# Optimization experiments

Measured on AMD Instinct MI355X. Metric: run time of the kernel, lower is better.

The kernel has to match this reference:

```python
import jax, jax.numpy as jnp
from jax import lax
import numpy as np

# ---- config (matches init_kwargs) ----
B, T, D_IN = 4, 2048, 513
NC = D_IN - 1                 # neural channels
N_DAYS, N_CLASSES = 24, 41
PATCH, STRIDE = 14, 4
T_OUT = (T - PATCH) // STRIDE + 1   # 509
D_MODEL = 512                 # n_units
PROJ = 4096
L = 5                         # n_layers
DSTATE, DCONV, HEADDIM = 64, 4, 64
DI = 2 * D_MODEL              # expand=2 -> d_inner
H = DI // HEADDIM             # 16 heads
CONVD = DI + 2 * DSTATE       # conv channels (x,B,C)
DINPROJ = 2 * DI + 2 * DSTATE + H
NM = 2 * L                    # fwd+bwd Mamba instances
EPS = 1e-5


def setup_inputs() -> dict:
    key = jax.random.key(0)
    ks = jax.random.split(key, 16)
    s = 0.02
    x = jax.random.normal(ks[0], (B, T, D_IN), jnp.float32)
    day_idx = jax.random.randint(ks[1], (B,), 0, N_DAYS)
    day_w = jnp.eye(NC)[None] + s * jax.random.normal(ks[2], (N_DAYS, NC, NC), jnp.float32)
    day_b = s * jax.random.normal(ks[3], (N_DAYS, NC), jnp.float32)
    w1 = s * jax.random.normal(ks[4], (PROJ, D_IN * PATCH), jnp.float32)
    b1 = jnp.zeros((PROJ,), jnp.float32)
    w2 = s * jax.random.normal(ks[5], (D_MODEL, PROJ), jnp.float32)
    b2 = jnp.zeros((D_MODEL,), jnp.float32)
    ln_w = jnp.ones((L, D_MODEL), jnp.float32)
    ln_b = jnp.zeros((L, D_MODEL), jnp.float32)
    m_in_w = s * jax.random.normal(ks[6], (NM, DINPROJ, D_MODEL), jnp.float32)
    m_conv_w = s * jax.random.normal(ks[7], (NM, CONVD, DCONV), jnp.float32)
    m_conv_b = jnp.zeros((NM, CONVD), jnp.float32)
    dt = jax.random.uniform(ks[8], (NM, H), jnp.float32, 0.025, 1.0)
    m_dt = jnp.log(jnp.expm1(dt)) + 1.0          # dt_bias with +1 short-memory bias
    m_Alog = jnp.tile(jnp.log(jnp.arange(1, H + 1, dtype=jnp.float32))[None], (NM, 1))
    m_D = jnp.ones((NM, H), jnp.float32)
    m_norm_w = jnp.ones((NM, DI), jnp.float32)
    m_out_w = s * jax.random.normal(ks[9], (NM, D_MODEL, DI), jnp.float32)
    out_w = s * jax.random.normal(ks[10], (N_CLASSES, D_MODEL), jnp.float32)
    out_b = jnp.zeros((N_CLASSES,), jnp.float32)
    return dict(x=x, day_idx=day_idx, day_w=day_w, day_b=day_b, w1=w1, b1=b1,
                w2=w2, b2=b2, ln_w=ln_w, ln_b=ln_b, m_in_w=m_in_w, m_conv_w=m_conv_w,
                m_conv_b=m_conv_b, m_dt=m_dt, m_Alog=m_Alog, m_D=m_D,
                m_norm_w=m_norm_w, m_out_w=m_out_w, out_w=out_w, out_b=out_b)


def _layernorm(x, w, b):
    mu = jnp.mean(x, -1, keepdims=True)
    v = jnp.mean((x - mu) ** 2, -1, keepdims=True)
    return (x - mu) * lax.rsqrt(v + EPS) * w + b


def _mamba2(x, in_w, conv_w, conv_b, dt_bias, A_log, Dp, norm_w, out_w):
    """Mamba2 forward: x [B,T,Dm] -> [B,T,Dm]. Sequential selective scan."""
    Bn, Tn, _ = x.shape
    zxbcdt = x @ in_w.T                                   # [B,T,DINPROJ]
    z = zxbcdt[..., :DI]
    xBC = zxbcdt[..., DI:DI + CONVD]
    dt = jax.nn.softplus(zxbcdt[..., DI + CONVD:] + dt_bias)  # [B,T,H]
    # causal depthwise conv over time
    xc = jnp.transpose(xBC, (0, 2, 1))                    # [B,C,T]
    xc = lax.conv_general_dilated(xc, conv_w[:, None, :], (1,), [(DCONV - 1, 0)],
                                  feature_group_count=CONVD)
    xBC = jax.nn.silu(jnp.transpose(xc, (0, 2, 1)) + conv_b)
    xs = xBC[..., :DI].reshape(Bn, Tn, H, HEADDIM)        # [B,T,H,P]
    Bm = xBC[..., DI:DI + DSTATE]                         # [B,T,N] (ngroups=1)
    Cm = xBC[..., DI + DSTATE:]                           # [B,T,N]
    A = -jnp.exp(A_log)                                   # [H]
    dA = jnp.exp(dt * A)                                  # [B,T,H]

    def step(h, inp):
        xt, bt, ct, dat, dtt = inp                        # [B,H,P],[B,N],[B,N],[B,H],[B,H]
        h = h * dat[:, :, None, None] + (dtt[:, :, None] * xt)[..., None] * bt[:, None, None, :]
        y = jnp.einsum('bhpn,bn->bhp', h, ct)
        return h, y

    h0 = jnp.zeros((Bn, H, HEADDIM, DSTATE), x.dtype)
    xsT = jnp.moveaxis(xs, 1, 0)
    _, ys = lax.scan(step, h0, (xsT, jnp.moveaxis(Bm, 1, 0), jnp.moveaxis(Cm, 1, 0),
                                jnp.moveaxis(dA, 1, 0), jnp.moveaxis(dt, 1, 0)))
    y = jnp.moveaxis(ys, 0, 1) + Dp[None, None, :, None] * xs
    y = y.reshape(Bn, Tn, DI)
    y = y * jax.nn.silu(z)                                # gated RMSNorm
    y = y * lax.rsqrt(jnp.mean(y * y, -1, keepdims=True) + EPS) * norm_w
    return y @ out_w.T


def reference(x, day_idx, day_w, day_b, w1, b1, w2, b2, ln_w, ln_b,
              m_in_w, m_conv_w, m_conv_b, m_dt, m_Alog, m_D, m_norm_w, m_out_w,
              out_w, out_b):
    xn, xt = x[..., :-1], x[..., -1:]
    W = day_w[day_idx]                                    # [B,NC,NC]
    bsel = day_b[day_idx][:, None, :]
    xn = jnp.einsum('btd,bdk->btk', xn, W) + bsel
    xn = xn / (1.0 + jnp.abs(xn))                         # Softsign
    h = jnp.concatenate([xn, xt], -1)                     # [B,T,D_IN]
    # patch unfold: [B,T_OUT,PATCH,D_IN] -> [B,T_OUT,PATCH*D_IN]
    idx = jnp.arange(T_OUT)[:, None] * STRIDE + jnp.arange(PATCH)[None, :]
    h = h[:, idx, :].reshape(B, T_OUT, PATCH * D_IN)
    # input projection with Softsign
    h = h @ w1.T + b1
    h = h / (1.0 + jnp.abs(h))
    h = h @ w2.T + b2                                     # [B,T_OUT,D_MODEL]
    for i in range(L):
        hn = _layernorm(h, ln_w[i], ln_b[i])
        f, bw = 2 * i, 2 * i + 1
        of = _mamba2(hn, m_in_w[f], m_conv_w[f], m_conv_b[f], m_dt[f], m_Alog[f],
                     m_D[f], m_norm_w[f], m_out_w[f])
        ob = _mamba2(jnp.flip(hn, 1), m_in_w[bw], m_conv_w[bw], m_conv_b[bw], m_dt[bw],
                     m_Alog[bw], m_D[bw], m_norm_w[bw], m_out_w[bw])
        h = h + of + jnp.flip(ob, 1)
    return h @ out_w.T + out_b                            # [B,T_OUT,N_CLASSES]
```

## Files before the change

### kernel.cpp

```cpp
#include <hip/hip_runtime.h>

#define TB 4
#define TT 2048
#define DIN 513
#define TOUT 509
#define M2 2036
#define DM 512
#define PR 4096
#define DIc 1024
#define Hh 16
#define CONVD 1152
#define DINP 2192
#define ZLD 4384
#define LC 128
#define NC 4
#define KW1 7182
#define KP1 7200

typedef __attribute__((ext_vector_type(8))) short s8v;
typedef __attribute__((ext_vector_type(4))) float f4v;

__device__ __forceinline__ short f2b(float f) {
    unsigned u = __float_as_uint(f);
    u += 0x7fffu + ((u >> 16) & 1u);
    return (short)(u >> 16);
}

__device__ __forceinline__ void gld16(const void* g, void* l) {
    __builtin_amdgcn_global_load_lds(
        (const __attribute__((address_space(1))) unsigned int*)g,
        (__attribute__((address_space(3))) unsigned int*)l, 16, 0, 0);
}
__device__ __forceinline__ void gld4(const void* g, void* l) {
    __builtin_amdgcn_global_load_lds(
        (const __attribute__((address_space(1))) unsigned int*)g,
        (__attribute__((address_space(3))) unsigned int*)l, 4, 0, 0);
}

__global__ __launch_bounds__(256) void day_gemm(const float* __restrict__ x,
                                                const int* __restrict__ day_idx,
                                                const float* __restrict__ day_w,
                                                const float* __restrict__ day_b,
                                                short* __restrict__ hfull) {
    int b = blockIdx.z;
    int day = day_idx[b];
    int n0 = blockIdx.x * 64, m0 = blockIdx.y * 64;
    int tid = threadIdx.x;
    __shared__ float As[16][68], Bs[16][68];
    float acc[4][4] = {};
    int tm = tid >> 4, tn = tid & 15;
    int lrow = tid >> 2, lk = (tid & 3) * 4;
    const float* Ab = x + ((size_t)b * TT + m0) * DIN;
    const float* Bb = day_w + (size_t)day * 512 * 512;
    for (int k0 = 0; k0 < 512; k0 += 16) {
        #pragma unroll
        for (int j = 0; j < 4; j++)
            As[lk + j][lrow] = Ab[(size_t)lrow * DIN + k0 + lk + j];
        int kb = tid >> 4; int nb = (tid & 15) * 4;
        #pragma unroll
        for (int j = 0; j < 4; j++)
            Bs[kb][nb + j] = Bb[(size_t)(k0 + kb) * 512 + n0 + nb + j];
        __syncthreads();
        #pragma unroll
        for (int kk = 0; kk < 16; kk++) {
            float4 av = *(const float4*)&As[kk][tm * 4];
            float4 bv = *(const float4*)&Bs[kk][tn * 4];
            float a[4] = {av.x, av.y, av.z, av.w};
            float bb2[4] = {bv.x, bv.y, bv.z, bv.w};
            #pragma unroll
            for (int i = 0; i < 4; i++)
                #pragma unroll
                for (int j = 0; j < 4; j++) acc[i][j] += a[i] * bb2[j];
        }
        __syncthreads();
    }
    #pragma unroll
    for (int i = 0; i < 4; i++) {
        int m = m0 + tm * 4 + i;
        #pragma unroll
        for (int j = 0; j < 4; j++) {
            int n = n0 + tn * 4 + j;
            float v = acc[i][j] + day_b[day * 512 + n];
            v = v / (1.f + fabsf(v));
            hfull[((size_t)b * TT + m) * DIN + n] = f2b(v);
        }
    }
}

__global__ void copy_xt(const float* __restrict__ x, short* __restrict__ hfull) {
    int idx = blockIdx.x * 256 + threadIdx.x;
    if (idx >= TB * TT) return;
    hfull[(size_t)idx * DIN + 512] = f2b(x[(size_t)idx * DIN + 512]);
}

__global__ void cvt_w1(const float* __restrict__ s, short* __restrict__ d) {
    long idx = (long)blockIdx.x * 256 + threadIdx.x;
    if (idx >= (long)4096 * 900) return;
    int row = (int)(idx / 900);
    int kc = (int)(idx % 900) * 8;
    const float* src = s + (long)row * KW1 + kc;
    short* dst = d + (long)row * KP1 + kc;
    if (kc + 8 <= KW1) {
        const float2* s2 = (const float2*)src;
        #pragma unroll
        for (int j = 0; j < 4; j++) {
            float2 u = s2[j];
            dst[2 * j] = f2b(u.x); dst[2 * j + 1] = f2b(u.y);
        }
    } else {
        #pragma unroll
        for (int j = 0; j < 8; j++)
            dst[j] = (kc + j < KW1) ? f2b(src[j]) : (short)0;
    }
}

__global__ void cvtk(const float* __restrict__ s, short* __restrict__ d, long n) {
    long i = ((long)blockIdx.x * 256 + threadIdx.x) * 4;
    if (i >= n) return;
    float4 v = *(const float4*)(s + i);
    d[i] = f2b(v.x); d[i + 1] = f2b(v.y); d[i + 2] = f2b(v.z); d[i + 3] = f2b(v.w);
}

__global__ void cvt_outw(const float* __restrict__ fw, const float* __restrict__ bw,
                         short* __restrict__ d) {
    long idx = (long)blockIdx.x * 256 + threadIdx.x;
    if (idx >= (long)512 * 512) return;
    long e = idx * 4;
    int n = (int)(e >> 11);
    int k = (int)(e & 2047);
    const float* src = (k < 1024) ? (fw + (long)n * 1024 + k)
                                  : (bw + (long)n * 1024 + (k - 1024));
    float4 v = *(const float4*)src;
    short* dst = d + e;
    dst[0] = f2b(v.x); dst[1] = f2b(v.y); dst[2] = f2b(v.z); dst[3] = f2b(v.w);
}

template <int ACT, int ACCUM, int OUTBF, int AW>
__global__ __launch_bounds__(256) void bgemm(const short* __restrict__ A,
                                             const short* __restrict__ Bw,
                                             const float* __restrict__ bias,
                                             void* __restrict__ Cout,
                                             int M, int N, int K,
                                             int rowDiv, long sOuter, long sInner, int ldc) {
    __shared__ short As[128 * 32];
    __shared__ short Bs[128 * 32];
    int m0 = blockIdx.y * 128, n0 = blockIdx.x * 128;
    int tid = threadIdx.x;
    int wave = tid >> 6, lane = tid & 63;
    int wm = (wave & 1) * 64, wn = (wave >> 1) * 64;
    int lm = lane & 15, quad = lane >> 4;

    const short* Ap[(AW == 4) ? 8 : 2];
    if constexpr (AW == 4) {
        int kcc = (lane & 15) * 2;
        #pragma unroll
        for (int c = 0; c < 8; c++) {
            int r = m0 + wave * 32 + c * 4 + (lane >> 4);
            r = min(r, M - 1);
            Ap[c] = A + (long)(r / rowDiv) * sOuter + (long)(r % rowDiv) * sInner + kcc;
        }
    } else {
        int kca = (lane & 3) * 8;
        int r0 = min(m0 + wave * 32 + (lane >> 2), M - 1);
        int r1 = min(m0 + wave * 32 + 16 + (lane >> 2), M - 1);
        Ap[0] = A + (long)(r0 / rowDiv) * sOuter + (long)(r0 % rowDiv) * sInner + kca;
        Ap[1] = A + (long)(r1 / rowDiv) * sOuter + (long)(r1 % rowDiv) * sInner + kca;
    }
    int kcb = (lane & 3) * 8;
    int b0 = min(n0 + wave * 32 + (lane >> 2), N - 1);
    int b1 = min(n0 + wave * 32 + 16 + (lane >> 2), N - 1);
    const short* Bp0 = Bw + (long)b0 * K + kcb;
    const short* Bp1 = Bw + (long)b1 * K + kcb;
    short* lA = As + wave * 1024;
    short* lB = Bs + wave * 1024;

    f4v acc[4][4];
    #pragma unroll
    for (int i = 0; i < 4; i++)
        #pragma unroll
        for (int j = 0; j < 4; j++) acc[i][j] = (f4v){0.f, 0.f, 0.f, 0.f};

    for (int k0 = 0; k0 < K; k0 += 32) {
        if constexpr (AW == 4) {
            #pragma unroll
            for (int c = 0; c < 8; c++)
                gld4(Ap[c] + k0, lA + c * 128);
        } else {
            gld16(Ap[0] + k0, lA);
            gld16(Ap[1] + k0, lA + 512);
        }
        gld16(Bp0 + k0, lB);
        gld16(Bp1 + k0, lB + 512);
        __syncthreads();
        s8v af[4], bf[4];
        #pragma unroll
        for (int i = 0; i < 4; i++)
            af[i] = *(const s8v*)&As[(wm + i * 16 + lm) * 32 + quad * 8];
        #pragma unroll
        for (int j = 0; j < 4; j++)
            bf[j] = *(const s8v*)&Bs[(wn + j * 16 + lm) * 32 + quad * 8];
        #pragma unroll
        for (int i = 0; i < 4; i++)
            #pragma unroll
            for (int j = 0; j < 4; j++)
                acc[i][j] = __builtin_amdgcn_mfma_f32_16x16x32_bf16(af[i], bf[j], acc[i][j], 0, 0, 0);
        __syncthreads();
    }

    #pragma unroll
    for (int i = 0; i < 4; i++) {
        #pragma unroll
        for (int e = 0; e < 4; e++) {
            int m = m0 + wm + i * 16 + quad * 4 + e;
            if (m >= M) continue;
            #pragma unroll
            for (int j = 0; j < 4; j++) {
                int n = n0 + wn + j * 16 + lm;
                if (n >= N) continue;
                float v = acc[i][j][e];
                if (bias) v += bias[n];
                if (ACT == 1) v = v / (1.f + fabsf(v));
                long ci = (long)m * ldc + n;
                if constexpr (OUTBF) {
                    ((short*)Cout)[ci] = f2b(v);
                } else {
                    float* Cf = (float*)Cout;
                    if constexpr (ACCUM) v += Cf[ci];
                    Cf[ci] = v;
                }
            }
        }
    }
}

__global__ __launch_bounds__(64) void ln_kernel(const float* __restrict__ h,
                                                const float* __restrict__ w,
                                                const float* __restrict__ bgain,
                                                short* __restrict__ hn) {
    int m = blockIdx.x, lane = threadIdx.x;
    const float* row = h + (size_t)m * DM;
    float v[8]; float s = 0.f;
    #pragma unroll
    for (int j = 0; j < 8; j++) { v[j] = row[lane + j * 64]; s += v[j]; }
    for (int o = 1; o < 64; o <<= 1) s += __shfl_xor(s, o);
    float mu = s * (1.f / DM);
    float var = 0.f;
    #pragma unroll
    for (int j = 0; j < 8; j++) { float d = v[j] - mu; var += d * d; }
    for (int o = 1; o < 64; o <<= 1) var += __shfl_xor(var, o);
    float inv = rsqrtf(var * (1.f / DM) + 1e-5f);
    #pragma unroll
    for (int j = 0; j < 8; j++) {
        int c = lane + j * 64;
        hn[(size_t)m * DM + c] = f2b((v[j] - mu) * inv * w[c] + bgain[c]);
    }
}

__global__ void conv_kernel(const float* __restrict__ zx2,
                            const float* __restrict__ cw,
                            const float* __restrict__ cb,
                            float* __restrict__ xbcc) {
    int idx = blockIdx.x * 256 + threadIdx.x;
    if (idx >= 2 * M2 * CONVD) return;
    int dir = idx / (M2 * CONVD);
    int r = idx - dir * (M2 * CONVD);
    int m = r / CONVD; int c = r - m * CONVD;
    int b = m / TOUT; int t = m - b * TOUT;
    float acc = cb[dir * CONVD + c];
    const float* w = cw + (size_t)(dir * CONVD + c) * 4;
    #pragma unroll
    for (int k = 0; k < 4; k++) {
        int tp = dir ? (t + 3 - k) : (t - 3 + k);
        if (tp >= 0 && tp < TOUT)
            acc += w[k] * zx2[(size_t)(b * TOUT + tp) * ZLD + dir * DINP + DIc + c];
    }
    xbcc[(size_t)idx] = acc / (1.f + expf(-acc));
}

__global__ void dt_kernel(const float* __restrict__ zx2,
                          const float* __restrict__ dtB,
                          const float* __restrict__ alog,
                          float* __restrict__ dtb, float* __restrict__ dab) {
    int idx = blockIdx.x * 256 + threadIdx.x;
    if (idx >= 2 * M2 * Hh) return;
    int dir = idx / (M2 * Hh);
    int r = idx - dir * (M2 * Hh);
    int m = r / Hh; int hh = r - m * Hh;
    float raw = zx2[(size_t)m * ZLD + dir * DINP + DIc + CONVD + hh] + dtB[dir * Hh + hh];
    float sp = raw > 20.f ? raw : log1pf(expf(raw));
    float A = -expf(alog[dir * Hh + hh]);
    dtb[idx] = sp;
    dab[idx] = expf(sp * A);
}

__global__ __launch_bounds__(64) void scan_local(const float* __restrict__ xbcc,
                                                 const float* __restrict__ dtb,
                                                 const float* __restrict__ dab,
                                                 const float* __restrict__ Dp_pair,
                                                 float* __restrict__ ybuf,
                                                 float* __restrict__ Hbuf,
                                                 float* __restrict__ Pcum) {
    int h = blockIdx.x & 15, chunk = blockIdx.x >> 4;
    int b = blockIdx.y, dir = blockIdx.z;
    int lane = threadIdx.x;
    int s0 = chunk * LC;
    int s1 = min(s0 + LC, TOUT);
    __shared__ __align__(16) float bsh[2][64];
    __shared__ __align__(16) float csh[2][64];
    float st[64];
    #pragma unroll
    for (int n = 0; n < 64; n++) st[n] = 0.f;
    float Dpv = Dp_pair[dir * Hh + h];
    const float* xb = xbcc + (size_t)dir * M2 * CONVD;
    long dtbase = (size_t)(dir * M2 + b * TOUT) * Hh + h;
    int id = (dir * TB + b) * Hh + h;
    float* pcm = Pcum + (size_t)id * TOUT;

    int tt0 = dir ? (TOUT - 1 - s0) : s0;
    const float* row0 = xb + (size_t)(b * TOUT + tt0) * CONVD;
    float bcur = row0[DIc + lane];
    float ccur = row0[DIc + 64 + lane];
    float xcur = row0[h * 64 + lane];
    float dtcur = dtb[dtbase + (long)tt0 * Hh];
    float dacur = dab[dtbase + (long)tt0 * Hh];
    float P = 1.f;

    for (int s = s0; s < s1; s++) {
        int pb = s & 1;
        bsh[pb][lane] = bcur;
        csh[pb][lane] = ccur;
        float xp = xcur, dtt = dtcur, da = dacur;
        __syncthreads();
        if (s + 1 < s1) {
            int tn = dir ? (TOUT - 1 - (s + 1)) : (s + 1);
            const float* rown = xb + (size_t)(b * TOUT + tn) * CONVD;
            bcur = rown[DIc + lane];
            ccur = rown[DIc + 64 + lane];
            xcur = rown[h * 64 + lane];
            dtcur = dtb[dtbase + (long)tn * Hh];
            dacur = dab[dtbase + (long)tn * Hh];
        }
        float common = dtt * xp;
        float y0 = 0.f, y1 = 0.f, y2 = 0.f, y3 = 0.f;
        #pragma unroll
        for (int n4 = 0; n4 < 16; n4++) {
            float4 bv = ((const float4*)bsh[pb])[n4];
            float4 cv = ((const float4*)csh[pb])[n4];
            int n = n4 * 4;
            st[n]     = st[n]     * da + common * bv.x; y0 += st[n]     * cv.x;
            st[n + 1] = st[n + 1] * da + common * bv.y; y1 += st[n + 1] * cv.y;
            st[n + 2] = st[n + 2] * da + common * bv.z; y2 += st[n + 2] * cv.z;
            st[n + 3] = st[n + 3] * da + common * bv.w; y3 += st[n + 3] * cv.w;
        }
        int tt = dir ? (TOUT - 1 - s) : s;
        int m = b * TOUT + tt;
        ybuf[((size_t)dir * M2 + m) * DIc + h * 64 + lane] = (y0 + y1) + (y2 + y3) + Dpv * xp;
        P *= da;
        if (lane == 0) pcm[s] = P;
    }
    float* Ho = Hbuf + (((size_t)id * NC + chunk) * 64 + lane) * 64;
    #pragma unroll
    for (int n4 = 0; n4 < 16; n4++) {
        ((float4*)Ho)[n4] = (float4){st[n4 * 4], st[n4 * 4 + 1], st[n4 * 4 + 2], st[n4 * 4 + 3]};
    }
}

__global__ __launch_bounds__(64) void scan_combine(float* __restrict__ Hbuf,
                                                   const float* __restrict__ Pcum) {
    int id = blockIdx.x;
    int lane = threadIdx.x;
    float Hin[64];
    #pragma unroll
    for (int n = 0; n < 64; n++) Hin[n] = 0.f;
    const float* pcm = Pcum + (size_t)id * TOUT;
    for (int c = 0; c < NC; c++) {
        float* Hp = Hbuf + (((size_t)id * NC + c) * 64 + lane) * 64;
        float Hout[64];
        #pragma unroll
        for (int n4 = 0; n4 < 16; n4++) {
            float4 v = ((const float4*)Hp)[n4];
            Hout[n4 * 4] = v.x; Hout[n4 * 4 + 1] = v.y;
            Hout[n4 * 4 + 2] = v.z; Hout[n4 * 4 + 3] = v.w;
        }
        #pragma unroll
        for (int n4 = 0; n4 < 16; n4++)
            ((float4*)Hp)[n4] = (float4){Hin[n4 * 4], Hin[n4 * 4 + 1], Hin[n4 * 4 + 2], Hin[n4 * 4 + 3]};
        int send = min((c + 1) * LC, TOUT) - 1;
        float Pe = pcm[send];
        #pragma unroll
        for (int n = 0; n < 64; n++) Hin[n] = Hout[n] + Pe * Hin[n];
    }
}

__global__ __launch_bounds__(64) void scan_fix(const float* __restrict__ xbcc,
                                               const float* __restrict__ Hbuf,
                                               const float* __restrict__ Pcum,
                                               float* __restrict__ ybuf) {
    int h = blockIdx.x & 15;
    int q = (blockIdx.x >> 4) & 3;
    int c = 1 + (blockIdx.x >> 6);
    int b = blockIdx.y, dir = blockIdx.z, lane = threadIdx.x;
    int s0 = c * LC;
    int s1 = min(s0 + LC, TOUT);
    int sa = s0 + q * (LC / 4);
    int se = min(sa + LC / 4, s1);
    if (sa >= se) return;
    int id = (dir * TB + b) * Hh + h;
    float Hr[64];
    const float* Hp = Hbuf + (((size_t)id * NC + c) * 64 + lane) * 64;
    #pragma unroll
    for (int n4 = 0; n4 < 16; n4++) {
        float4 v = ((const float4*)Hp)[n4];
        Hr[n4 * 4] = v.x; Hr[n4 * 4 + 1] = v.y; Hr[n4 * 4 + 2] = v.z; Hr[n4 * 4 + 3] = v.w;
    }
    const float* pcm = Pcum + (size_t)id * TOUT;
    const float* xb = xbcc + (size_t)dir * M2 * CONVD;
    for (int s = sa; s < se; s++) {
        int tt = dir ? (TOUT - 1 - s) : s;
        const float4* crow = (const float4*)(xb + (size_t)(b * TOUT + tt) * CONVD + DIc + 64);
        float acc = 0.f;
        #pragma unroll
        for (int n4 = 0; n4 < 16; n4++) {
            float4 cv = crow[n4];
            acc += Hr[n4 * 4] * cv.x + Hr[n4 * 4 + 1] * cv.y
                 + Hr[n4 * 4 + 2] * cv.z + Hr[n4 * 4 + 3] * cv.w;
        }
        size_t yi = ((size_t)dir * M2 + b * TOUT + tt) * DIc + h * 64 + lane;
        ybuf[yi] += pcm[s] * acc;
    }
}

__global__ __launch_bounds__(64) void grms_kernel(const float* __restrict__ ybuf,
                                                  const float* __restrict__ zx2,
                                                  const float* __restrict__ nw,
                                                  short* __restrict__ yo) {
    int m = blockIdx.x, dir = blockIdx.y, lane = threadIdx.x;
    const float* y = ybuf + ((size_t)dir * M2 + m) * DIc;
    const float* z = zx2 + (size_t)m * ZLD + dir * DINP;
    float g[16]; float ss = 0.f;
    #pragma unroll
    for (int j = 0; j < 16; j++) {
        int c = lane + j * 64;
        float zv = z[c];
        float gv = y[c] * (zv / (1.f + expf(-zv)));
        g[j] = gv; ss += gv * gv;
    }
    for (int o = 1; o < 64; o <<= 1) ss += __shfl_xor(ss, o);
    float sc = rsqrtf(ss * (1.f / DIc) + 1e-5f);
    #pragma unroll
    for (int j = 0; j < 16; j++) {
        int c = lane + j * 64;
        yo[(size_t)m * (2 * DIc) + dir * DIc + c] = f2b(g[j] * sc * nw[dir * DIc + c]);
    }
}

__global__ __launch_bounds__(64) void outk(const float* __restrict__ h,
                                           const float* __restrict__ ow,
                                           const float* __restrict__ ob,
                                           float* __restrict__ out) {
    int m = blockIdx.x, lane = threadIdx.x;
    __shared__ float hs[DM];
    #pragma unroll
    for (int j = 0; j < 8; j++) hs[lane + j * 64] = h[(size_t)m * DM + lane + j * 64];
    __syncthreads();
    if (lane < 41) {
        float acc = ob[lane];
        for (int d = 0; d < DM; d++) acc += hs[d] * ow[lane * DM + d];
        out[(size_t)m * 41 + lane] = acc;
    }
}

extern "C" void kernel_launch(void* const* d_in, const int* in_sizes, int n_in,
                              void* d_out, int out_size, void* d_ws, size_t ws_size,
                              hipStream_t stream) {
    const float* x        = (const float*)d_in[0];
    const int*   day_idx  = (const int*)d_in[1];
    const float* day_w    = (const float*)d_in[2];
    const float* day_b    = (const float*)d_in[3];
    const float* w1       = (const float*)d_in[4];
    const float* b1       = (const float*)d_in[5];
    const float* w2       = (const float*)d_in[6];
    const float* b2       = (const float*)d_in[7];
    const float* ln_w     = (const float*)d_in[8];
    const float* ln_b     = (const float*)d_in[9];
    const float* m_in_w   = (const float*)d_in[10];
    const float* m_conv_w = (const float*)d_in[11];
    const float* m_conv_b = (const float*)d_in[12];
    const float* m_dt     = (const float*)d_in[13];
    const float* m_Alog   = (const float*)d_in[14];
    const float* m_D      = (const float*)d_in[15];
    const float* m_norm_w = (const float*)d_in[16];
    const float* m_out_w  = (const float*)d_in[17];
    const float* out_w    = (const float*)d_in[18];
    const float* out_b    = (const float*)d_in[19];

    float* ws = (float*)d_ws;
    float* zx2  = ws;
    float* xbcc = ws + 8925824;
    short* ybf  = (short*)(ws + 8925824);
    float* ybuf = ws + 13616768;
    float* Hbuf = ws + 17786496;
    float* Pcum = ws + 19883648;
    float* dtb  = ws + 19948800;
    float* dab  = ws + 20013952;
    short* inwb = (short*)(ws + 20079104);
    short* outwb= (short*)(ws + 21201408);
    short* hfb  = (short*)ws;
    short* B1   = (short*)(ws + 2103296);
    short* h1b  = (short*)(ws + 16848896);
    short* w2b  = (short*)(ws + 21018624);
    float* hbuf = ws + 22067200;
    short* hnb  = (short*)(ws + 23109632);

    day_gemm<<<dim3(8, 32, 4), 256, 0, stream>>>(x, day_idx, day_w, day_b, hfb);
    copy_xt<<<32, 256, 0, stream>>>(x, hfb);
    cvt_w1<<<14400, 256, 0, stream>>>(w1, B1);
    cvtk<<<2048, 256, 0, stream>>>(w2, w2b, (long)512 * PR);
    bgemm<1, 0, 1, 4><<<dim3(32, 16), 256, 0, stream>>>(hfb, B1, b1, h1b,
                                                        M2, PR, KP1, TOUT, (long)TT * DIN, (long)4 * DIN, PR);
    bgemm<0, 0, 0, 16><<<dim3(4, 16), 256, 0, stream>>>(h1b, w2b, b2, hbuf,
                                                        M2, DM, PR, 1, (long)PR, 0L, DM);
    for (int i = 0; i < 5; i++) {
        ln_kernel<<<M2, 64, 0, stream>>>(hbuf, ln_w + i * DM, ln_b + i * DM, hnb);
        cvtk<<<2192, 256, 0, stream>>>(m_in_w + (size_t)2 * i * DINP * DM, inwb, (long)2 * DINP * DM);
        bgemm<0, 0, 0, 16><<<dim3(35, 16), 256, 0, stream>>>(hnb, inwb, nullptr, zx2,
                                                             M2, ZLD, DM, 1, (long)DM, 0L, ZLD);
        conv_kernel<<<(2 * M2 * CONVD + 255) / 256, 256, 0, stream>>>(
            zx2, m_conv_w + (size_t)2 * i * CONVD * 4, m_conv_b + (size_t)2 * i * CONVD, xbcc);
        dt_kernel<<<(2 * M2 * Hh + 255) / 256, 256, 0, stream>>>(
            zx2, m_dt + 2 * i * Hh, m_Alog + 2 * i * Hh, dtb, dab);
        scan_local<<<dim3(Hh * NC, TB, 2), 64, 0, stream>>>(xbcc, dtb, dab, m_D + 2 * i * Hh,
                                                            ybuf, Hbuf, Pcum);
        scan_combine<<<128, 64, 0, stream>>>(Hbuf, Pcum);
        scan_fix<<<dim3(Hh * 4 * (NC - 1), TB, 2), 64, 0, stream>>>(xbcc, Hbuf, Pcum, ybuf);
        grms_kernel<<<dim3(M2, 2), 64, 0, stream>>>(ybuf, zx2, m_norm_w + (size_t)2 * i * DIc, ybf);
        cvt_outw<<<1024, 256, 0, stream>>>(m_out_w + (size_t)(2 * i) * DM * DIc,
                                           m_out_w + (size_t)(2 * i + 1) * DM * DIc, outwb);
        bgemm<0, 1, 0, 16><<<dim3(4, 16), 256, 0, stream>>>(ybf, outwb, nullptr, hbuf,
                                                            M2, DM, 2 * DIc, 1, (long)(2 * DIc), 0L, DM);
    }
    outk<<<M2, 64, 0, stream>>>(hbuf, out_w, out_b, (float*)d_out);
}
```

Before: 2.224 ms.

## Materialize patch matrix, split-K atomic GEMMs, XCD-aware block remap

Replaces the 4-byte gather loads of the unfolded patch operand with an explicit padded patch matrix, so the first projection GEMM can use 16-byte global-to-LDS loads. The w1 conversion and GEMM are split into two halves to reuse a smaller workspace. The 512-wide GEMMs (w2 and the Mamba out-projection) switch to split-K with atomic float adds to fill more compute units; the bias is prefilled and the residual is accumulated through the atomics. All GEMMs also remap block IDs so that neighbouring tiles land on the same XCD for cache locality. This adds extra memory traffic for the expanded patches, and atomic accumulation makes the summation order nondeterministic.

```diff
diff --git a/kernel.cpp b/kernel.cpp
--- a/kernel.cpp
+++ b/kernel.cpp
@@ -31,11 +31,6 @@
         (const __attribute__((address_space(1))) unsigned int*)g,
         (__attribute__((address_space(3))) unsigned int*)l, 16, 0, 0);
 }
-__device__ __forceinline__ void gld4(const void* g, void* l) {
-    __builtin_amdgcn_global_load_lds(
-        (const __attribute__((address_space(1))) unsigned int*)g,
-        (__attribute__((address_space(3))) unsigned int*)l, 4, 0, 0);
-}
 
 __global__ __launch_bounds__(256) void day_gemm(const float* __restrict__ x,
                                                 const int* __restrict__ day_idx,
@@ -93,9 +88,20 @@
     hfull[(size_t)idx * DIN + 512] = f2b(x[(size_t)idx * DIN + 512]);
 }
 
-__global__ void cvt_w1(const float* __restrict__ s, short* __restrict__ d) {
+__global__ __launch_bounds__(256) void expand_patches(const short* __restrict__ hfb,
+                                                      short* __restrict__ Apad) {
+    int m = blockIdx.x;
+    int b = m / TOUT, t0 = m - b * TOUT;
+    const short* src = hfb + ((size_t)b * TT + (size_t)t0 * 4) * DIN;
+    short* dst = Apad + (size_t)m * KP1;
+    int tid = threadIdx.x;
+    for (int k = tid; k < KW1; k += 256) dst[k] = src[k];
+    if (tid < KP1 - KW1) dst[KW1 + tid] = 0;
+}
+
+__global__ void cvt_w1(const float* __restrict__ s, short* __restrict__ d, int rows) {
     long idx = (long)blockIdx.x * 256 + threadIdx.x;
-    if (idx >= (long)4096 * 900) return;
+    if (idx >= (long)rows * 900) return;
     int row = (int)(idx / 900);
     int kc = (int)(idx % 900) * 8;
     const float* src = s + (long)row * KW1 + kc;
@@ -135,7 +141,13 @@
     dst[0] = f2b(v.x); dst[1] = f2b(v.y); dst[2] = f2b(v.z); dst[3] = f2b(v.w);
 }
 
-template <int ACT, int ACCUM, int OUTBF, int AW>
+__global__ void fillb(float* __restrict__ dst, const float* __restrict__ b, int total, int N) {
+    int idx = blockIdx.x * 256 + threadIdx.x;
+    if (idx >= total) return;
+    dst[idx] = b[idx & (N - 1)];
+}
+
+template <int ACT, int ACCUM, int OUTBF, int ATOMIC>
 __global__ __launch_bounds__(256) void bgemm(const short* __restrict__ A,
                                              const short* __restrict__ Bw,
                                              const float* __restrict__ bias,
@@ -144,33 +156,28 @@
                                              int rowDiv, long sOuter, long sInner, int ldc) {
     __shared__ short As[128 * 32];
     __shared__ short Bs[128 * 32];
-    int m0 = blockIdx.y * 128, n0 = blockIdx.x * 128;
+    int nwg = gridDim.x * gridDim.y;
+    int orig = blockIdx.y * gridDim.x + blockIdx.x;
+    int q = nwg >> 3, rr = nwg & 7;
+    int xcd = orig & 7, ii = orig >> 3;
+    int wg = (xcd < rr ? xcd * (q + 1) : rr * (q + 1) + (xcd - rr) * q) + ii;
+    int bx = wg % gridDim.x, by = wg / gridDim.x;
+    int m0 = by * 128, n0 = bx * 128;
+
     int tid = threadIdx.x;
     int wave = tid >> 6, lane = tid & 63;
     int wm = (wave & 1) * 64, wn = (wave >> 1) * 64;
     int lm = lane & 15, quad = lane >> 4;
 
-    const short* Ap[(AW == 4) ? 8 : 2];
-    if constexpr (AW == 4) {
-        int kcc = (lane & 15) * 2;
-        #pragma unroll
-        for (int c = 0; c < 8; c++) {
-            int r = m0 + wave * 32 + c * 4 + (lane >> 4);
-            r = min(r, M - 1);
-            Ap[c] = A + (long)(r / rowDiv) * sOuter + (long)(r % rowDiv) * sInner + kcc;
-        }
-    } else {
-        int kca = (lane & 3) * 8;
-        int r0 = min(m0 + wave * 32 + (lane >> 2), M - 1);
-        int r1 = min(m0 + wave * 32 + 16 + (lane >> 2), M - 1);
-        Ap[0] = A + (long)(r0 / rowDiv) * sOuter + (long)(r0 % rowDiv) * sInner + kca;
-        Ap[1] = A + (long)(r1 / rowDiv) * sOuter + (long)(r1 % rowDiv) * sInner + kca;
-    }
-    int kcb = (lane & 3) * 8;
+    int kca = (lane & 3) * 8;
+    int r0 = min(m0 + wave * 32 + (lane >> 2), M - 1);
+    int r1 = min(m0 + wave * 32 + 16 + (lane >> 2), M - 1);
+    const short* Ap0 = A + (long)(r0 / rowDiv) * sOuter + (long)(r0 % rowDiv) * sInner + kca;
+    const short* Ap1 = A + (long)(r1 / rowDiv) * sOuter + (long)(r1 % rowDiv) * sInner + kca;
     int b0 = min(n0 + wave * 32 + (lane >> 2), N - 1);
     int b1 = min(n0 + wave * 32 + 16 + (lane >> 2), N - 1);
-    const short* Bp0 = Bw + (long)b0 * K + kcb;
-    const short* Bp1 = Bw + (long)b1 * K + kcb;
+    const short* Bp0 = Bw + (long)b0 * K + kca;
+    const short* Bp1 = Bw + (long)b1 * K + kca;
     short* lA = As + wave * 1024;
     short* lB = Bs + wave * 1024;
 
@@ -180,15 +187,11 @@
         #pragma unroll
         for (int j = 0; j < 4; j++) acc[i][j] = (f4v){0.f, 0.f, 0.f, 0.f};
 
-    for (int k0 = 0; k0 < K; k0 += 32) {
-        if constexpr (AW == 4) {
-            #pragma unroll
-            for (int c = 0; c < 8; c++)
-                gld4(Ap[c] + k0, lA + c * 128);
-        } else {
-            gld16(Ap[0] + k0, lA);
-            gld16(Ap[1] + k0, lA + 512);
-        }
+    int kper = K, kbeg = 0;
+    if constexpr (ATOMIC) { kper = K / (int)gridDim.z; kbeg = blockIdx.z * kper; }
+    for (int k0 = kbeg; k0 < kbeg + kper; k0 += 32) {
+        gld16(Ap0 + k0, lA);
+        gld16(Ap1 + k0, lA + 512);
         gld16(Bp0 + k0, lB);
         gld16(Bp1 + k0, lB + 512);
         __syncthreads();
@@ -223,6 +226,8 @@
                 long ci = (long)m * ldc + n;
                 if constexpr (OUTBF) {
                     ((short*)Cout)[ci] = f2b(v);
+                } else if constexpr (ATOMIC) {
+                    unsafeAtomicAdd(&((float*)Cout)[ci], v);
                 } else {
                     float* Cf = (float*)Cout;
                     if constexpr (ACCUM) v += Cf[ci];
@@ -495,6 +500,13 @@
     const float* out_b    = (const float*)d_in[19];
 
     float* ws = (float*)d_ws;
+    short* hfb  = (short*)ws;
+    short* Apad = (short*)(ws + 2101248);
+    short* B1h  = (short*)(ws + 9430848);
+    short* h1b  = (short*)(ws + 16803648);
+    short* w2b  = (short*)(ws + 20973376);
+    float* hbuf = ws + 22021952;
+    short* hnb  = (short*)(ws + 23064384);
     float* zx2  = ws;
     float* xbcc = ws + 8925824;
     short* ybf  = (short*)(ws + 8925824);
@@ -505,26 +517,25 @@
     float* dab  = ws + 20013952;
     short* inwb = (short*)(ws + 20079104);
     short* outwb= (short*)(ws + 21201408);
-    short* hfb  = (short*)ws;
-    short* B1   = (short*)(ws + 2103296);
-    short* h1b  = (short*)(ws + 16848896);
-    short* w2b  = (short*)(ws + 21018624);
-    float* hbuf = ws + 22067200;
-    short* hnb  = (short*)(ws + 23109632);
 
     day_gemm<<<dim3(8, 32, 4), 256, 0, stream>>>(x, day_idx, day_w, day_b, hfb);
     copy_xt<<<32, 256, 0, stream>>>(x, hfb);
-    cvt_w1<<<14400, 256, 0, stream>>>(w1, B1);
+    expand_patches<<<M2, 256, 0, stream>>>(hfb, Apad);
     cvtk<<<2048, 256, 0, stream>>>(w2, w2b, (long)512 * PR);
-    bgemm<1, 0, 1, 4><<<dim3(32, 16), 256, 0, stream>>>(hfb, B1, b1, h1b,
-                                                        M2, PR, KP1, TOUT, (long)TT * DIN, (long)4 * DIN, PR);
-    bgemm<0, 0, 0, 16><<<dim3(4, 16), 256, 0, stream>>>(h1b, w2b, b2, hbuf,
-                                                        M2, DM, PR, 1, (long)PR, 0L, DM);
+    for (int half = 0; half < 2; half++) {
+        cvt_w1<<<7200, 256, 0, stream>>>(w1 + (size_t)half * 2048 * KW1, B1h, 2048);
+        bgemm<1, 0, 1, 0><<<dim3(16, 16), 256, 0, stream>>>(
+            Apad, B1h, b1 + half * 2048, h1b + half * 2048,
+            M2, 2048, KP1, 1, (long)KP1, 0L, PR);
+    }
+    fillb<<<(M2 * DM + 255) / 256, 256, 0, stream>>>(hbuf, b2, M2 * DM, DM);
+    bgemm<0, 0, 0, 1><<<dim3(4, 16, 4), 256, 0, stream>>>(h1b, w2b, nullptr, hbuf,
+                                                          M2, DM, PR, 1, (long)PR, 0L, DM);
     for (int i = 0; i < 5; i++) {
         ln_kernel<<<M2, 64, 0, stream>>>(hbuf, ln_w + i * DM, ln_b + i * DM, hnb);
         cvtk<<<2192, 256, 0, stream>>>(m_in_w + (size_t)2 * i * DINP * DM, inwb, (long)2 * DINP * DM);
-        bgemm<0, 0, 0, 16><<<dim3(35, 16), 256, 0, stream>>>(hnb, inwb, nullptr, zx2,
-                                                             M2, ZLD, DM, 1, (long)DM, 0L, ZLD);
+        bgemm<0, 0, 0, 0><<<dim3(35, 16), 256, 0, stream>>>(hnb, inwb, nullptr, zx2,
+                                                            M2, ZLD, DM, 1, (long)DM, 0L, ZLD);
         conv_kernel<<<(2 * M2 * CONVD + 255) / 256, 256, 0, stream>>>(
             zx2, m_conv_w + (size_t)2 * i * CONVD * 4, m_conv_b + (size_t)2 * i * CONVD, xbcc);
         dt_kernel<<<(2 * M2 * Hh + 255) / 256, 256, 0, stream>>>(
@@ -536,8 +547,8 @@
         grms_kernel<<<dim3(M2, 2), 64, 0, stream>>>(ybuf, zx2, m_norm_w + (size_t)2 * i * DIc, ybf);
         cvt_outw<<<1024, 256, 0, stream>>>(m_out_w + (size_t)(2 * i) * DM * DIc,
                                            m_out_w + (size_t)(2 * i + 1) * DM * DIc, outwb);
-        bgemm<0, 1, 0, 16><<<dim3(4, 16), 256, 0, stream>>>(ybf, outwb, nullptr, hbuf,
-                                                            M2, DM, 2 * DIc, 1, (long)(2 * DIc), 0L, DM);
+        bgemm<0, 0, 0, 1><<<dim3(4, 16, 4), 256, 0, stream>>>(ybf, outwb, nullptr, hbuf,
+                                                              M2, DM, 2 * DIc, 1, (long)(2 * DIc), 0L, DM);
     }
     outk<<<M2, 64, 0, stream>>>(hbuf, out_w, out_b, (float*)d_out);
 }
```

After: 2.180 ms. 1.02x faster.
